# Kernel optimization log

Measured on AMD Instinct MI355X. Metric: run time of the kernel, lower is better.

## Reference

```python
import jax, jax.numpy as jnp
import numpy as np

N_NODES = 50000
EMBED_DIM = 512
N_EDGES = 800000
NEG_SLOPE = 0.01  # nn.LeakyReLU default


def setup_inputs() -> dict:
    key = jax.random.key(0)
    k1, k2, k3 = jax.random.split(key, 3)
    X = jax.random.normal(k1, (N_NODES, EMBED_DIM), dtype=jnp.float32)
    # Glorot-ish scale for the GCNConv weight
    W = jax.random.normal(k2, (EMBED_DIM, EMBED_DIM), dtype=jnp.float32) / np.sqrt(EMBED_DIM)
    b = jnp.zeros((EMBED_DIM,), dtype=jnp.float32)
    edge_index = jax.random.randint(k3, (2, N_EDGES), 0, N_NODES, dtype=jnp.int32)
    return {"X": X, "W": W, "b": b, "edge_index": edge_index}


def reference(X, W, b, edge_index):
    N = X.shape[0]
    # GCNConv: add self-loops, symmetric normalization deg^-1/2 A deg^-1/2
    loop = jnp.arange(N, dtype=edge_index.dtype)
    src = jnp.concatenate([edge_index[0], loop])  # [E+N]
    dst = jnp.concatenate([edge_index[1], loop])  # [E+N]
    deg = jax.ops.segment_sum(jnp.ones_like(dst, dtype=X.dtype), dst, num_segments=N)
    dinv = jnp.where(deg > 0, jax.lax.rsqrt(deg), 0.0)  # deg^{-1/2}, inf->0
    norm = dinv[src] * dinv[dst]                         # [E+N]
    H = X @ W                                            # [N, D] dense GEMM
    msgs = H[src] * norm[:, None]                        # [E+N, D] gathered messages
    out = jax.ops.segment_sum(msgs, dst, num_segments=N) + b
    # LeakyReLU activation; Dropout is identity in eval mode
    return jnp.where(out >= 0, out, NEG_SLOPE * out)
```

## Files before the change

### kernel.cpp

```cpp
#include <hip/hip_runtime.h>
#include <cstdint>
#include <cstddef>

#define DFEAT 512
#define BM 128
#define BN 128
#define BK 32

typedef __attribute__((ext_vector_type(8))) short bf16x8;
typedef __attribute__((ext_vector_type(4))) float f32x4;

#define GLOBAL_AS __attribute__((address_space(1)))
#define LDS_AS __attribute__((address_space(3)))

__device__ __forceinline__ unsigned short f2bf(float f) {
  unsigned u = __float_as_uint(f);
  u = u + 0x7fffu + ((u >> 16) & 1u);
  return (unsigned short)(u >> 16);
}

__device__ __forceinline__ float bf2f_lo(unsigned u) { return __uint_as_float(u << 16); }
__device__ __forceinline__ float bf2f_hi(unsigned u) { return __uint_as_float(u & 0xffff0000u); }

__device__ __forceinline__ void gl_lds16(const void* g, void* l) {
  __builtin_amdgcn_global_load_lds((const GLOBAL_AS unsigned int*)g,
                                   (LDS_AS unsigned int*)l, 16, 0, 0);
}

__global__ void k_count(const int* __restrict__ dst, int* __restrict__ deg8,
                        int E, int N) {
  const int i = blockIdx.x * 256 + threadIdx.x;
  if (i < E) {
    const int d = __builtin_nontemporal_load(dst + i);
    atomicAdd(&deg8[(size_t)(blockIdx.x & 7) * N + d], 1);
  }
}

__global__ void k_reduce(const int* __restrict__ deg8, int* __restrict__ deg, int N) {
  const int i = blockIdx.x * 256 + threadIdx.x;
  if (i >= N) return;
  int s = 0;
#pragma unroll
  for (int x = 0; x < 8; ++x) s += deg8[(size_t)x * N + i];
  deg[i] = s;
}

__global__ void k_cast(const float* __restrict__ W, unsigned short* __restrict__ Wt,
                       const float* __restrict__ X, unsigned short* __restrict__ Xb,
                       int total8) {
  int b = blockIdx.x;
  if (b < 1024) {
    int i = b * 256 + threadIdx.x;
    int k = i >> 9, n = i & 511;
    Wt[(size_t)n * DFEAT + k] = f2bf(W[i]);
    return;
  }
  b -= 1024;
  int i = b * 256 + threadIdx.x;
  if (i >= total8) return;
  const f32x4 a = __builtin_nontemporal_load(reinterpret_cast<const f32x4*>(X + (size_t)i * 8));
  const f32x4 c = __builtin_nontemporal_load(reinterpret_cast<const f32x4*>(X + (size_t)i * 8 + 4));
  uint4 o;
  o.x = (unsigned)f2bf(a[0]) | ((unsigned)f2bf(a[1]) << 16);
  o.y = (unsigned)f2bf(a[2]) | ((unsigned)f2bf(a[3]) << 16);
  o.z = (unsigned)f2bf(c[0]) | ((unsigned)f2bf(c[1]) << 16);
  o.w = (unsigned)f2bf(c[2]) | ((unsigned)f2bf(c[3]) << 16);
  *reinterpret_cast<uint4*>(Xb + (size_t)i * 8) = o;
}

__global__ __launch_bounds__(1024) void k_scan(const int* __restrict__ deg,
                                               int* __restrict__ rowStart,
                                               int* __restrict__ fillPos, int N) {
  const int t = threadIdx.x;
  const int base = blockIdx.x * 1024;
  __shared__ int sm[1024];
  int pre = 0;
  for (int i = t; i < base; i += 1024) pre += deg[i] + 1;
  sm[t] = pre;
  __syncthreads();
  for (int d = 512; d > 0; d >>= 1) {
    if (t < d) sm[t] += sm[t + d];
    __syncthreads();
  }
  const int blockBase = sm[0];
  __syncthreads();
  const int idx = base + t;
  int v = (idx < N) ? (deg[idx] + 1) : 0;
  sm[t] = v;
  __syncthreads();
  for (int d = 1; d < 1024; d <<= 1) {
    const int o = (t >= d) ? sm[t - d] : 0;
    __syncthreads();
    sm[t] += o;
    __syncthreads();
  }
  if (idx < N) {
    const int ex = blockBase + sm[t] - v;
    rowStart[idx] = ex;
    fillPos[idx] = ex;
    if (idx == N - 1) rowStart[N] = ex + v;
  }
}

__global__ void k_fill(const int* __restrict__ src, const int* __restrict__ dst,
                       int* __restrict__ fillPos, int2* __restrict__ cw,
                       const int* __restrict__ deg, int E, int N) {
  int i = blockIdx.x * blockDim.x + threadIdx.x;
  if (i >= E + N) return;
  int d, s;
  if (i < E) { d = dst[i]; s = src[i]; }
  else       { d = i - E; s = d; }
  int pos = atomicAdd(&fillPos[d], 1);
  int2 q; q.x = s; q.y = __float_as_int(rsqrtf((float)(deg[s] + 1)));
  cw[pos] = q;
}

template <bool TAIL>
__device__ __forceinline__ void agg8(const unsigned short* __restrict__ Xb,
                                     const int2* __restrict__ cw,
                                     int p, int e, int lane, float* acc) {
  int2 q[8];
#pragma unroll
  for (int i = 0; i < 8; ++i) {
    int pi = p + i;
    if (TAIL) pi = (pi < e) ? pi : (e - 1);
    q[i] = cw[pi];
  }
  uint4 v[8];
#pragma unroll
  for (int i = 0; i < 8; ++i)
    v[i] = *reinterpret_cast<const uint4*>(Xb + (size_t)q[i].x * DFEAT + lane * 8);
#pragma unroll
  for (int i = 0; i < 8; ++i) {
    float w = __int_as_float(q[i].y);
    if (TAIL) w = (p + i < e) ? w : 0.0f;
    acc[0] = fmaf(w, bf2f_lo(v[i].x), acc[0]); acc[1] = fmaf(w, bf2f_hi(v[i].x), acc[1]);
    acc[2] = fmaf(w, bf2f_lo(v[i].y), acc[2]); acc[3] = fmaf(w, bf2f_hi(v[i].y), acc[3]);
    acc[4] = fmaf(w, bf2f_lo(v[i].z), acc[4]); acc[5] = fmaf(w, bf2f_hi(v[i].z), acc[5]);
    acc[6] = fmaf(w, bf2f_lo(v[i].w), acc[6]); acc[7] = fmaf(w, bf2f_hi(v[i].w), acc[7]);
  }
}

__global__ __launch_bounds__(256) void k_aggregate(const unsigned short* __restrict__ Xb,
                                                   const int2* __restrict__ cw,
                                                   const int* __restrict__ rowStart,
                                                   unsigned short* __restrict__ Y,
                                                   int N, int rowOff) {
  const int row = rowOff + blockIdx.x * 4 + (threadIdx.x >> 6);
  const int lane = threadIdx.x & 63;
  float acc[8] = {0.f, 0.f, 0.f, 0.f, 0.f, 0.f, 0.f, 0.f};
  if (row < N) {
    const int s = rowStart[row], e = rowStart[row + 1];
    int p = s;
    for (; p + 8 <= e; p += 8) agg8<false>(Xb, cw, p, e, lane, acc);
    if (p < e) agg8<true>(Xb, cw, p, e, lane, acc);
    const float sc = rsqrtf((float)(e - s));
#pragma unroll
    for (int j = 0; j < 8; ++j) acc[j] *= sc;
  }
  uint4 o;
  o.x = (unsigned)f2bf(acc[0]) | ((unsigned)f2bf(acc[1]) << 16);
  o.y = (unsigned)f2bf(acc[2]) | ((unsigned)f2bf(acc[3]) << 16);
  o.z = (unsigned)f2bf(acc[4]) | ((unsigned)f2bf(acc[5]) << 16);
  o.w = (unsigned)f2bf(acc[6]) | ((unsigned)f2bf(acc[7]) << 16);
  *reinterpret_cast<uint4*>(Y + (size_t)row * DFEAT + lane * 8) = o;
}

__global__ __launch_bounds__(256) void k_gemm(const unsigned short* __restrict__ Y,
                                              const unsigned short* __restrict__ Wt,
                                              const float* __restrict__ bias,
                                              float* __restrict__ out, int M) {
  __shared__ unsigned short As[BM * BK];
  __shared__ unsigned short Bs[BN * BK];
  const int tid = threadIdx.x;
  const int lane = tid & 63;
  const int wave = tid >> 6;
  const int l16 = lane & 15;
  const int quad = lane >> 4;
  const int wm = (wave >> 1) * 64;
  const int wn = (wave & 1) * 64;

  const int nwg = gridDim.x;
  const int q8 = nwg >> 3, r8 = nwg & 7;
  const int xcd = blockIdx.x & 7, loc = blockIdx.x >> 3;
  const int wg = (xcd < r8 ? xcd * (q8 + 1) : r8 * (q8 + 1) + (xcd - r8) * q8) + loc;
  const int m0 = (wg >> 2) * BM;
  const int n0 = (wg & 3) * BN;

  f32x4 acc[4][4];
#pragma unroll
  for (int mi = 0; mi < 4; ++mi)
#pragma unroll
    for (int ni = 0; ni < 4; ++ni) { f32x4 z = {0.f, 0.f, 0.f, 0.f}; acc[mi][ni] = z; }

  const int ci0 = wave * 64 + lane;
  const int ci1 = 256 + ci0;
  const int ra0 = ci0 >> 2, ka0 = (((ci0 & 3) - (ra0 >> 1)) & 3) * 8;
  const int ra1 = ci1 >> 2, ka1 = (((ci1 & 3) - (ra1 >> 1)) & 3) * 8;

  const unsigned short* Ag0 = Y + (size_t)(m0 + ra0) * DFEAT + ka0;
  const unsigned short* Ag1 = Y + (size_t)(m0 + ra1) * DFEAT + ka1;
  const unsigned short* Bg0 = Wt + (size_t)(n0 + ra0) * DFEAT + ka0;
  const unsigned short* Bg1 = Wt + (size_t)(n0 + ra1) * DFEAT + ka1;
  unsigned short* La0 = As + ci0 * 8;
  unsigned short* La1 = As + ci1 * 8;
  unsigned short* Lb0 = Bs + ci0 * 8;
  unsigned short* Lb1 = Bs + ci1 * 8;

  const int rotA = (quad + ((wm + l16) >> 1)) & 3;
  const int rotB = (quad + ((wn + l16) >> 1)) & 3;
  const unsigned short* AsRd = As + (wm + l16) * BK + rotA * 8;
  const unsigned short* BsRd = Bs + (wn + l16) * BK + rotB * 8;

  for (int kk = 0; kk < DFEAT; kk += BK) {
    gl_lds16(Ag0 + kk, La0);
    gl_lds16(Ag1 + kk, La1);
    gl_lds16(Bg0 + kk, Lb0);
    gl_lds16(Bg1 + kk, Lb1);
    __syncthreads();
    bf16x8 av[4], bv[4];
#pragma unroll
    for (int mi = 0; mi < 4; ++mi)
      av[mi] = *reinterpret_cast<const bf16x8*>(AsRd + mi * 16 * BK);
#pragma unroll
    for (int ni = 0; ni < 4; ++ni)
      bv[ni] = *reinterpret_cast<const bf16x8*>(BsRd + ni * 16 * BK);
#pragma unroll
    for (int mi = 0; mi < 4; ++mi)
#pragma unroll
      for (int ni = 0; ni < 4; ++ni)
        acc[mi][ni] = __builtin_amdgcn_mfma_f32_16x16x32_bf16(av[mi], bv[ni], acc[mi][ni], 0, 0, 0);
    __syncthreads();
  }

  float bvals[4];
#pragma unroll
  for (int ni = 0; ni < 4; ++ni) bvals[ni] = bias[n0 + wn + 16 * ni + l16];

#pragma unroll
  for (int mi = 0; mi < 4; ++mi) {
#pragma unroll
    for (int r = 0; r < 4; ++r) {
      int row = m0 + wm + 16 * mi + quad * 4 + r;
      if (row < M) {
#pragma unroll
        for (int ni = 0; ni < 4; ++ni) {
          float v = acc[mi][ni][r] + bvals[ni];
          v = (v >= 0.f) ? v : 0.01f * v;
          out[(size_t)row * DFEAT + n0 + wn + 16 * ni + l16] = v;
        }
      }
    }
  }
}

extern "C" void kernel_launch(void* const* d_in, const int* in_sizes, int n_in,
                              void* d_out, int out_size, void* d_ws, size_t ws_size,
                              hipStream_t stream) {
  const float* X = (const float*)d_in[0];
  const float* W = (const float*)d_in[1];
  const float* b = (const float*)d_in[2];
  const int* ei  = (const int*)d_in[3];
  const int D = DFEAT;
  const int N = in_sizes[0] / D;
  const int E = in_sizes[3] / 2;
  const int* src = ei;
  const int* dst = ei + E;
  float* out = (float*)d_out;

  uintptr_t p = (uintptr_t)d_ws;
  auto carve = [&](size_t bytes) -> void* {
    uintptr_t r = p;
    p += (bytes + 255) & ~(size_t)255;
    return (void*)r;
  };
  int*   deg8     = (int*)carve(sizeof(int) * (size_t)N * 8);
  int*   deg      = (int*)carve(sizeof(int) * (size_t)N);
  int*   rowStart = (int*)carve(sizeof(int) * (size_t)(N + 1));
  int*   fillPos  = (int*)carve(sizeof(int) * (size_t)N);
  int2*  cw       = (int2*)carve(sizeof(int2) * (size_t)(E + N));
  unsigned short* Wt = (unsigned short*)carve(sizeof(unsigned short) * (size_t)D * D);
  const int Mtiles = (N + BM - 1) / BM;
  const int Mpad = Mtiles * BM;
  unsigned short* Y  = (unsigned short*)carve(sizeof(unsigned short) * (size_t)Mpad * D);

  unsigned short* Xb = (unsigned short*)d_out;

  const int total8 = N * D / 8;
  const int xb = (total8 + 255) / 256;
  const int quarter = ((Mpad / 4 + 3) & ~3);

  hipMemsetAsync(deg8, 0, sizeof(int) * (size_t)N * 8, stream);
  hipLaunchKernelGGL(k_count,  dim3((E + 255) / 256), dim3(256), 0, stream, dst, deg8, E, N);
  hipLaunchKernelGGL(k_reduce, dim3((N + 255) / 256), dim3(256), 0, stream, deg8, deg, N);
  hipLaunchKernelGGL(k_scan,   dim3((N + 1023) / 1024), dim3(1024), 0, stream,
                     deg, rowStart, fillPos, N);
  hipLaunchKernelGGL(k_fill,   dim3((E + N + 255) / 256), dim3(256), 0, stream,
                     src, dst, fillPos, cw, deg, E, N);
  hipLaunchKernelGGL(k_cast,   dim3(1024 + xb), dim3(256), 0, stream, W, Wt, X, Xb, total8);
  for (int qq = 0; qq < 4; ++qq) {
    const int ro = qq * quarter;
    const int nr = (qq == 3) ? (Mpad - 3 * quarter) : quarter;
    hipLaunchKernelGGL(k_aggregate, dim3(nr / 4), dim3(256), 0, stream,
                       Xb, cw, rowStart, Y, N, ro);
  }
  hipLaunchKernelGGL(k_gemm,   dim3(Mtiles * 4), dim3(256), 0, stream, Y, Wt, b, out, N);
}
```

Measured before the change: 442.6 us.

## Fuse degree reduce into scan, merge fill with cast, handle self-loops implicitly

Folds the per-partition degree reduction into the scan kernel and merges the CSR fill kernel with the bf16 cast kernel into one launch. Self-loops are no longer stored in the CSR. The aggregate kernel adds each row's own contribution directly and uses deg+1 for normalisation. Edge-list loads become nontemporal, and the aggregate runs as a single launch instead of four. This cuts launch count, CSR size and atomics, at the cost of a scan that re-reads eight partitions per prefix element.

```diff
diff --git a/kernel.cpp b/kernel.cpp
--- a/kernel.cpp
+++ b/kernel.cpp
@@ -36,27 +36,78 @@
   }
 }
 
-__global__ void k_reduce(const int* __restrict__ deg8, int* __restrict__ deg, int N) {
-  const int i = blockIdx.x * 256 + threadIdx.x;
-  if (i >= N) return;
-  int s = 0;
-#pragma unroll
-  for (int x = 0; x < 8; ++x) s += deg8[(size_t)x * N + i];
-  deg[i] = s;
-}
-
-__global__ void k_cast(const float* __restrict__ W, unsigned short* __restrict__ Wt,
-                       const float* __restrict__ X, unsigned short* __restrict__ Xb,
-                       int total8) {
+__global__ __launch_bounds__(1024) void k_scan(const int* __restrict__ deg8,
+                                               int* __restrict__ deg,
+                                               int* __restrict__ rowStart,
+                                               int* __restrict__ fillPos, int N) {
+  const int t = threadIdx.x;
+  const int base = blockIdx.x * 1024;
+  __shared__ int sm[1024];
+  int pre = 0;
+  for (int i = t; i < base; i += 1024) {
+    int s = 0;
+#pragma unroll
+    for (int x = 0; x < 8; ++x) s += deg8[(size_t)x * N + i];
+    pre += s;
+  }
+  sm[t] = pre;
+  __syncthreads();
+  for (int d = 512; d > 0; d >>= 1) {
+    if (t < d) sm[t] += sm[t + d];
+    __syncthreads();
+  }
+  const int blockBase = sm[0];
+  __syncthreads();
+  const int idx = base + t;
+  int v = 0;
+  if (idx < N) {
+#pragma unroll
+    for (int x = 0; x < 8; ++x) v += deg8[(size_t)x * N + idx];
+    deg[idx] = v;
+  }
+  sm[t] = v;
+  __syncthreads();
+  for (int d = 1; d < 1024; d <<= 1) {
+    const int o = (t >= d) ? sm[t - d] : 0;
+    __syncthreads();
+    sm[t] += o;
+    __syncthreads();
+  }
+  if (idx < N) {
+    const int ex = blockBase + sm[t] - v;
+    rowStart[idx] = ex;
+    fillPos[idx] = ex;
+    if (idx == N - 1) rowStart[N] = ex + v;
+  }
+}
+
+__global__ void k_fillcast(const int* __restrict__ src, const int* __restrict__ dst,
+                           int* __restrict__ fillPos, int2* __restrict__ cw,
+                           const int* __restrict__ deg, int E,
+                           const float* __restrict__ W, unsigned short* __restrict__ Wt,
+                           const float* __restrict__ X, unsigned short* __restrict__ Xb,
+                           int total8) {
+  const int fb = (E + 255) >> 8;
   int b = blockIdx.x;
+  if (b < fb) {
+    const int i = b * 256 + threadIdx.x;
+    if (i < E) {
+      const int d = dst[i], s = src[i];
+      const int pos = atomicAdd(&fillPos[d], 1);
+      int2 q; q.x = s; q.y = __float_as_int(rsqrtf((float)(deg[s] + 1)));
+      cw[pos] = q;
+    }
+    return;
+  }
+  b -= fb;
   if (b < 1024) {
-    int i = b * 256 + threadIdx.x;
-    int k = i >> 9, n = i & 511;
+    const int i = b * 256 + threadIdx.x;
+    const int k = i >> 9, n = i & 511;
     Wt[(size_t)n * DFEAT + k] = f2bf(W[i]);
     return;
   }
   b -= 1024;
-  int i = b * 256 + threadIdx.x;
+  const int i = b * 256 + threadIdx.x;
   if (i >= total8) return;
   const f32x4 a = __builtin_nontemporal_load(reinterpret_cast<const f32x4*>(X + (size_t)i * 8));
   const f32x4 c = __builtin_nontemporal_load(reinterpret_cast<const f32x4*>(X + (size_t)i * 8 + 4));
@@ -68,71 +119,24 @@
   *reinterpret_cast<uint4*>(Xb + (size_t)i * 8) = o;
 }
 
-__global__ __launch_bounds__(1024) void k_scan(const int* __restrict__ deg,
-                                               int* __restrict__ rowStart,
-                                               int* __restrict__ fillPos, int N) {
-  const int t = threadIdx.x;
-  const int base = blockIdx.x * 1024;
-  __shared__ int sm[1024];
-  int pre = 0;
-  for (int i = t; i < base; i += 1024) pre += deg[i] + 1;
-  sm[t] = pre;
-  __syncthreads();
-  for (int d = 512; d > 0; d >>= 1) {
-    if (t < d) sm[t] += sm[t + d];
-    __syncthreads();
-  }
-  const int blockBase = sm[0];
-  __syncthreads();
-  const int idx = base + t;
-  int v = (idx < N) ? (deg[idx] + 1) : 0;
-  sm[t] = v;
-  __syncthreads();
-  for (int d = 1; d < 1024; d <<= 1) {
-    const int o = (t >= d) ? sm[t - d] : 0;
-    __syncthreads();
-    sm[t] += o;
-    __syncthreads();
-  }
-  if (idx < N) {
-    const int ex = blockBase + sm[t] - v;
-    rowStart[idx] = ex;
-    fillPos[idx] = ex;
-    if (idx == N - 1) rowStart[N] = ex + v;
-  }
-}
-
-__global__ void k_fill(const int* __restrict__ src, const int* __restrict__ dst,
-                       int* __restrict__ fillPos, int2* __restrict__ cw,
-                       const int* __restrict__ deg, int E, int N) {
-  int i = blockIdx.x * blockDim.x + threadIdx.x;
-  if (i >= E + N) return;
-  int d, s;
-  if (i < E) { d = dst[i]; s = src[i]; }
-  else       { d = i - E; s = d; }
-  int pos = atomicAdd(&fillPos[d], 1);
-  int2 q; q.x = s; q.y = __float_as_int(rsqrtf((float)(deg[s] + 1)));
-  cw[pos] = q;
-}
-
 template <bool TAIL>
 __device__ __forceinline__ void agg8(const unsigned short* __restrict__ Xb,
                                      const int2* __restrict__ cw,
                                      int p, int e, int lane, float* acc) {
-  int2 q[8];
+  unsigned long long q[8];
 #pragma unroll
   for (int i = 0; i < 8; ++i) {
     int pi = p + i;
     if (TAIL) pi = (pi < e) ? pi : (e - 1);
-    q[i] = cw[pi];
+    q[i] = __builtin_nontemporal_load(reinterpret_cast<const unsigned long long*>(cw + pi));
   }
   uint4 v[8];
 #pragma unroll
   for (int i = 0; i < 8; ++i)
-    v[i] = *reinterpret_cast<const uint4*>(Xb + (size_t)q[i].x * DFEAT + lane * 8);
+    v[i] = *reinterpret_cast<const uint4*>(Xb + (size_t)(unsigned)q[i] * DFEAT + lane * 8);
 #pragma unroll
   for (int i = 0; i < 8; ++i) {
-    float w = __int_as_float(q[i].y);
+    float w = __uint_as_float((unsigned)(q[i] >> 32));
     if (TAIL) w = (p + i < e) ? w : 0.0f;
     acc[0] = fmaf(w, bf2f_lo(v[i].x), acc[0]); acc[1] = fmaf(w, bf2f_hi(v[i].x), acc[1]);
     acc[2] = fmaf(w, bf2f_lo(v[i].y), acc[2]); acc[3] = fmaf(w, bf2f_hi(v[i].y), acc[3]);
@@ -144,17 +148,21 @@
 __global__ __launch_bounds__(256) void k_aggregate(const unsigned short* __restrict__ Xb,
                                                    const int2* __restrict__ cw,
                                                    const int* __restrict__ rowStart,
-                                                   unsigned short* __restrict__ Y,
-                                                   int N, int rowOff) {
-  const int row = rowOff + blockIdx.x * 4 + (threadIdx.x >> 6);
+                                                   unsigned short* __restrict__ Y, int N) {
+  const int row = blockIdx.x * 4 + (threadIdx.x >> 6);
   const int lane = threadIdx.x & 63;
   float acc[8] = {0.f, 0.f, 0.f, 0.f, 0.f, 0.f, 0.f, 0.f};
   if (row < N) {
     const int s = rowStart[row], e = rowStart[row + 1];
+    const float sc = rsqrtf((float)(e - s + 1));
+    const uint4 v0 = *reinterpret_cast<const uint4*>(Xb + (size_t)row * DFEAT + lane * 8);
+    acc[0] = sc * bf2f_lo(v0.x); acc[1] = sc * bf2f_hi(v0.x);
+    acc[2] = sc * bf2f_lo(v0.y); acc[3] = sc * bf2f_hi(v0.y);
+    acc[4] = sc * bf2f_lo(v0.z); acc[5] = sc * bf2f_hi(v0.z);
+    acc[6] = sc * bf2f_lo(v0.w); acc[7] = sc * bf2f_hi(v0.w);
     int p = s;
     for (; p + 8 <= e; p += 8) agg8<false>(Xb, cw, p, e, lane, acc);
     if (p < e) agg8<true>(Xb, cw, p, e, lane, acc);
-    const float sc = rsqrtf((float)(e - s));
 #pragma unroll
     for (int j = 0; j < 8; ++j) acc[j] *= sc;
   }
@@ -278,7 +286,7 @@
   int*   deg      = (int*)carve(sizeof(int) * (size_t)N);
   int*   rowStart = (int*)carve(sizeof(int) * (size_t)(N + 1));
   int*   fillPos  = (int*)carve(sizeof(int) * (size_t)N);
-  int2*  cw       = (int2*)carve(sizeof(int2) * (size_t)(E + N));
+  int2*  cw       = (int2*)carve(sizeof(int2) * (size_t)E);
   unsigned short* Wt = (unsigned short*)carve(sizeof(unsigned short) * (size_t)D * D);
   const int Mtiles = (N + BM - 1) / BM;
   const int Mpad = Mtiles * BM;
@@ -287,22 +295,16 @@
   unsigned short* Xb = (unsigned short*)d_out;
 
   const int total8 = N * D / 8;
+  const int fb = (E + 255) / 256;
   const int xb = (total8 + 255) / 256;
-  const int quarter = ((Mpad / 4 + 3) & ~3);
 
   hipMemsetAsync(deg8, 0, sizeof(int) * (size_t)N * 8, stream);
-  hipLaunchKernelGGL(k_count,  dim3((E + 255) / 256), dim3(256), 0, stream, dst, deg8, E, N);
-  hipLaunchKernelGGL(k_reduce, dim3((N + 255) / 256), dim3(256), 0, stream, deg8, deg, N);
-  hipLaunchKernelGGL(k_scan,   dim3((N + 1023) / 1024), dim3(1024), 0, stream,
-                     deg, rowStart, fillPos, N);
-  hipLaunchKernelGGL(k_fill,   dim3((E + N + 255) / 256), dim3(256), 0, stream,
-                     src, dst, fillPos, cw, deg, E, N);
-  hipLaunchKernelGGL(k_cast,   dim3(1024 + xb), dim3(256), 0, stream, W, Wt, X, Xb, total8);
-  for (int qq = 0; qq < 4; ++qq) {
-    const int ro = qq * quarter;
-    const int nr = (qq == 3) ? (Mpad - 3 * quarter) : quarter;
-    hipLaunchKernelGGL(k_aggregate, dim3(nr / 4), dim3(256), 0, stream,
-                       Xb, cw, rowStart, Y, N, ro);
-  }
-  hipLaunchKernelGGL(k_gemm,   dim3(Mtiles * 4), dim3(256), 0, stream, Y, Wt, b, out, N);
-}
+  hipLaunchKernelGGL(k_count,    dim3((E + 255) / 256), dim3(256), 0, stream, dst, deg8, E, N);
+  hipLaunchKernelGGL(k_scan,     dim3((N + 1023) / 1024), dim3(1024), 0, stream,
+                     deg8, deg, rowStart, fillPos, N);
+  hipLaunchKernelGGL(k_fillcast, dim3(fb + 1024 + xb), dim3(256), 0, stream,
+                     src, dst, fillPos, cw, deg, E, W, Wt, X, Xb, total8);
+  hipLaunchKernelGGL(k_aggregate, dim3(Mpad / 4), dim3(256), 0, stream,
+                     Xb, cw, rowStart, Y, N);
+  hipLaunchKernelGGL(k_gemm,     dim3(Mtiles * 4), dim3(256), 0, stream, Y, Wt, b, out, N);
+}
```

After: 435.0 us. No clear change (-1.7%).
